# Optimization experiments

Measured on AMD Instinct MI355X. Metric: run time of the kernel, lower is better.

The kernel has to match this reference:

```python
import jax, jax.numpy as jnp
import numpy as np

N_NODES = 50000
N_EDGES = 800000
IN_C, HID_C, OUT_C = 128, 64, 40


def setup_inputs() -> dict:
    key = jax.random.key(0)
    ks = jax.random.split(key, 8)
    x = jax.random.normal(ks[0], (N_NODES, IN_C), dtype=jnp.float32)
    edge_index = jax.random.randint(ks[1], (2, N_EDGES), 0, N_NODES, dtype=jnp.int32)
    # Glorot-style init for the three GCNConv linear layers (bias zero as in PyG default reset)
    def glorot(k, fan_in, fan_out):
        lim = jnp.sqrt(6.0 / (fan_in + fan_out)).astype(jnp.float32)
        return jax.random.uniform(k, (fan_in, fan_out), dtype=jnp.float32, minval=-lim, maxval=lim)
    return {
        "x": x,
        "edge_index": edge_index,
        "W1": glorot(ks[2], IN_C, HID_C), "b1": jnp.zeros((HID_C,), jnp.float32),
        "W2": glorot(ks[3], HID_C, HID_C), "b2": jnp.zeros((HID_C,), jnp.float32),
        "W3": glorot(ks[4], HID_C, OUT_C), "b3": jnp.zeros((OUT_C,), jnp.float32),
    }


def _gcn_norm(edge_index, num_nodes):
    # PyG gcn_norm: add self-loops (weight 1), symmetric D^-1/2 (A+I) D^-1/2.
    loop = jnp.arange(num_nodes, dtype=edge_index.dtype)
    row = jnp.concatenate([edge_index[0], loop])  # source
    col = jnp.concatenate([edge_index[1], loop])  # target
    w = jnp.ones(row.shape[0], dtype=jnp.float32)
    deg = jax.ops.segment_sum(w, col, num_segments=num_nodes)
    dinv = jnp.where(deg > 0, jax.lax.rsqrt(deg), 0.0)
    norm = dinv[row] * w * dinv[col]  # [E+N]
    return row, col, norm


def _gcn_conv(x, row, col, norm, W, b):
    h = x @ W                         # linear first, as in PyG GCNConv
    msg = h[row] * norm[:, None]      # gather + scale  [E+N, F]
    agg = jax.ops.segment_sum(msg, col, num_segments=x.shape[0])
    return agg + b


def reference(x, edge_index, W1, b1, W2, b2, W3, b3):
    row, col, norm = _gcn_norm(edge_index, x.shape[0])
    h = jax.nn.relu(_gcn_conv(x, row, col, norm, W1, b1))   # dropout: eval-mode identity
    h = jax.nn.relu(_gcn_conv(h, row, col, norm, W2, b2))
    h = _gcn_conv(h, row, col, norm, W3, b3)
    return jax.nn.log_softmax(h, axis=-1)
```

## Files before the change

### kernel.cpp

```cpp
#include <hip/hip_runtime.h>
#include <hip/hip_bf16.h>
#include <math.h>


#define BSHIFT 10
#define CHUNK 2048
#define CAP 24576

__global__ __launch_bounds__(64) void tinyzero_kernel(int* __restrict__ p) {
  p[threadIdx.x] = 0;
}


__global__ __launch_bounds__(256) void bucketA_kernel(const int* __restrict__ row,
                                                      const int* __restrict__ col,
                                                      int* __restrict__ bcursor,
                                                      int2* __restrict__ tmp, int e) {
  __shared__ int bcnt[64], bstart[64], bbase[64];
  __shared__ int2 stage[CHUNK];
  int tid = threadIdx.x;
  int base = blockIdx.x * CHUNK;
  int cnt = e - base;
  if (cnt > CHUNK) cnt = CHUNK;
  if (tid < 64) bcnt[tid] = 0;
  __syncthreads();

  int2 ed[CHUNK / 256];
  int rk[CHUNK / 256];
#pragma unroll
  for (int k = 0; k < CHUNK / 256; ++k) {
    int j = tid + k * 256;
    if (j < cnt) {
      int c = col[base + j], r = row[base + j];
      ed[k] = make_int2(c, r);
      rk[k] = atomicAdd(&bcnt[c >> BSHIFT], 1);
    }
  }
  __syncthreads();
  if (tid < 64) {
    int v = bcnt[tid];
    int run = v;
#pragma unroll
    for (int off = 1; off < 64; off <<= 1) {
      int t = __shfl_up(run, off);
      if (tid >= off) run += t;
    }
    bstart[tid] = run - v;
    if (v > 0) bbase[tid] = atomicAdd(&bcursor[tid], v);
  }
  __syncthreads();
#pragma unroll
  for (int k = 0; k < CHUNK / 256; ++k) {
    int j = tid + k * 256;
    if (j < cnt) stage[bstart[ed[k].x >> BSHIFT] + rk[k]] = ed[k];
  }
  __syncthreads();
  for (int s = tid; s < cnt; s += 256) {
    int2 ev = stage[s];
    int b = ev.x >> BSHIFT;
    tmp[(size_t)b * CAP + bbase[b] + (s - bstart[b])] = ev;
  }
}


__global__ __launch_bounds__(256) void scatterB_kernel(const int2* __restrict__ tmp,
                                                       const int* __restrict__ bcursor,
                                                       int4* __restrict__ meta,
                                                       float* __restrict__ dinv,
                                                       int* __restrict__ csr, int n) {
  __shared__ int cnt[1 << BSHIFT];
  __shared__ int part[256];
  int tid = threadIdx.x;
  int b = blockIdx.x;
  int node0 = b << BSHIFT;
  int m = bcursor[b];
  const int2* src = tmp + (size_t)b * CAP;

  for (int t = tid; t < (1 << BSHIFT); t += 256) cnt[t] = 0;
  __syncthreads();
  for (int i = tid; i < m; i += 256)
    atomicAdd(&cnt[src[i].x & ((1 << BSHIFT) - 1)], 1);
  __syncthreads();

  int c0 = cnt[tid * 4 + 0], c1 = cnt[tid * 4 + 1];
  int c2 = cnt[tid * 4 + 2], c3 = cnt[tid * 4 + 3];
  int lsum = c0 + c1 + c2 + c3;
  part[tid] = lsum;
  __syncthreads();
#pragma unroll
  for (int off = 1; off < 256; off <<= 1) {
    int t = (tid >= off) ? part[tid - off] : 0;
    __syncthreads();
    part[tid] += t;
    __syncthreads();
  }
  int e0 = (tid == 0 ? 0 : part[tid - 1]);
  int e1 = e0 + c0, e2 = e1 + c1, e3 = e2 + c2;
  int base = b * CAP;

  int nd = node0 + tid * 4;
  if (nd + 0 < n) { float d = rsqrtf((float)(c0 + 1)); meta[nd + 0] = make_int4(base + e0, c0, __float_as_int(d), 0); dinv[nd + 0] = d; }
  if (nd + 1 < n) { float d = rsqrtf((float)(c1 + 1)); meta[nd + 1] = make_int4(base + e1, c1, __float_as_int(d), 0); dinv[nd + 1] = d; }
  if (nd + 2 < n) { float d = rsqrtf((float)(c2 + 1)); meta[nd + 2] = make_int4(base + e2, c2, __float_as_int(d), 0); dinv[nd + 2] = d; }
  if (nd + 3 < n) { float d = rsqrtf((float)(c3 + 1)); meta[nd + 3] = make_int4(base + e3, c3, __float_as_int(d), 0); dinv[nd + 3] = d; }
  __syncthreads();
  cnt[tid * 4 + 0] = e0; cnt[tid * 4 + 1] = e1;
  cnt[tid * 4 + 2] = e2; cnt[tid * 4 + 3] = e3;
  __syncthreads();

  for (int i = tid; i < m; i += 256) {
    int2 ev = src[i];
    int pos = atomicAdd(&cnt[ev.x & ((1 << BSHIFT) - 1)], 1);
    csr[base + pos] = ev.y;
  }
}


template <int K, int F>
__global__ __launch_bounds__(256) void gemm_kernel(const float* __restrict__ X,
                                                   const float* __restrict__ W,
                                                   const float* __restrict__ dinv,
                                                   __hip_bfloat16* __restrict__ Y, int n) {
  __shared__ float xs[16][K];
  int tid = threadIdx.x;
  int node0 = blockIdx.x * 16;
  constexpr int KV = K / 4;
  const float4* X4 = (const float4*)X;
  for (int i = tid; i < 16 * KV; i += 256) {
    int r = i / KV, c = i % KV;
    int nd = node0 + r;
    float4 v = make_float4(0.f, 0.f, 0.f, 0.f);
    if (nd < n) v = X4[(size_t)nd * KV + c];
    ((float4*)&xs[r][0])[c] = v;
  }
  __syncthreads();
  int g = tid >> 6, lane = tid & 63;
  if (lane < F) {
    float acc0 = 0.f, acc1 = 0.f, acc2 = 0.f, acc3 = 0.f;
#pragma unroll 8
    for (int k = 0; k < K; ++k) {
      float w = W[k * F + lane];
      acc0 += xs[g * 4 + 0][k] * w;
      acc1 += xs[g * 4 + 1][k] * w;
      acc2 += xs[g * 4 + 2][k] * w;
      acc3 += xs[g * 4 + 3][k] * w;
    }
    float accs[4] = {acc0, acc1, acc2, acc3};
#pragma unroll
    for (int j = 0; j < 4; ++j) {
      int nd = node0 + g * 4 + j;
      if (nd < n) Y[(size_t)nd * F + lane] = __float2bfloat16(accs[j] * dinv[nd]);
    }
  }
}


__device__ __forceinline__ float bflo(unsigned int u) {
  return __uint_as_float(u << 16);
}
__device__ __forceinline__ float bfhi(unsigned int u) {
  return __uint_as_float(u & 0xffff0000u);
}

template <int F, int MODE>
__global__ __launch_bounds__(256) void agg_kernel(const unsigned short* __restrict__ Hs,
                                                  const int* __restrict__ csr,
                                                  const int4* __restrict__ meta,
                                                  const float* __restrict__ bias,
                                                  float* __restrict__ Y, int n) {
  constexpr int FQ = F / 4;
  int wv = (blockIdx.x * 256 + threadIdx.x) >> 6;
  int lane = threadIdx.x & 63;
  int half = lane >> 5;
  int l32 = lane & 31;
  int sub = l32 >> 4;
  int fid = lane & 15;
  int node = wv * 2 + half;
  if (node >= n) return;
  bool activeF = (FQ == 16) || (fid < FQ);
  int hbase = 32 * half;

  int4 mt = meta[node];
  int s = mt.x, e = mt.x + mt.y;
  float di = __int_as_float(mt.z);

  float a0 = 0.f, a1 = 0.f, a2 = 0.f, a3 = 0.f;
  if (sub == 0 && activeF) {
    uint2 u = *(const uint2*)(Hs + (size_t)node * F + 4 * fid);
    a0 = bflo(u.x); a1 = bfhi(u.x); a2 = bflo(u.y); a3 = bfhi(u.y);
  }

  for (int base = s; base < e; base += 32) {
    int rem = e - base;
    int cnt = rem < 32 ? rem : 32;
    int p = csr[base + (l32 < cnt ? l32 : 0)];
    int j = 0;
    for (; j + 8 <= cnt; j += 8) {
      int r0 = __shfl(p, j + 0 + sub + hbase);
      int r1 = __shfl(p, j + 2 + sub + hbase);
      int r2 = __shfl(p, j + 4 + sub + hbase);
      int r3 = __shfl(p, j + 6 + sub + hbase);
      if (activeF) {
        uint2 u0 = *(const uint2*)(Hs + (size_t)r0 * F + 4 * fid);
        uint2 u1 = *(const uint2*)(Hs + (size_t)r1 * F + 4 * fid);
        uint2 u2 = *(const uint2*)(Hs + (size_t)r2 * F + 4 * fid);
        uint2 u3 = *(const uint2*)(Hs + (size_t)r3 * F + 4 * fid);
        a0 += bflo(u0.x); a1 += bfhi(u0.x); a2 += bflo(u0.y); a3 += bfhi(u0.y);
        a0 += bflo(u1.x); a1 += bfhi(u1.x); a2 += bflo(u1.y); a3 += bfhi(u1.y);
        a0 += bflo(u2.x); a1 += bfhi(u2.x); a2 += bflo(u2.y); a3 += bfhi(u2.y);
        a0 += bflo(u3.x); a1 += bfhi(u3.x); a2 += bflo(u3.y); a3 += bfhi(u3.y);
      }
    }
    for (; j < cnt; j += 2) {
      int idx = j + sub;
      int r = __shfl(p, (idx < cnt ? idx : j) + hbase);
      if (activeF && idx < cnt) {
        uint2 u = *(const uint2*)(Hs + (size_t)r * F + 4 * fid);
        a0 += bflo(u.x); a1 += bfhi(u.x); a2 += bflo(u.y); a3 += bfhi(u.y);
      }
    }
  }

  a0 += __shfl_xor(a0, 16);
  a1 += __shfl_xor(a1, 16);
  a2 += __shfl_xor(a2, 16);
  a3 += __shfl_xor(a3, 16);

  if (MODE == 0) {
    if (sub == 0 && activeF) {
      float4 bv = *(const float4*)(bias + 4 * fid);
      float v0 = a0 * di + bv.x, v1 = a1 * di + bv.y;
      float v2 = a2 * di + bv.z, v3 = a3 * di + bv.w;
      v0 = v0 > 0.f ? v0 : 0.f;
      v1 = v1 > 0.f ? v1 : 0.f;
      v2 = v2 > 0.f ? v2 : 0.f;
      v3 = v3 > 0.f ? v3 : 0.f;
      *(float4*)(Y + (size_t)node * F + 4 * fid) = make_float4(v0, v1, v2, v3);
    }
  } else {
    float v0 = -INFINITY, v1 = -INFINITY, v2 = -INFINITY, v3 = -INFINITY;
    if (activeF) {
      float4 bv = *(const float4*)(bias + 4 * fid);
      v0 = a0 * di + bv.x; v1 = a1 * di + bv.y;
      v2 = a2 * di + bv.z; v3 = a3 * di + bv.w;
    }
    float m = fmaxf(fmaxf(v0, v1), fmaxf(v2, v3));
#pragma unroll
    for (int off = 8; off; off >>= 1) m = fmaxf(m, __shfl_xor(m, off));
    float ex = 0.f;
    if (activeF)
      ex = expf(v0 - m) + expf(v1 - m) + expf(v2 - m) + expf(v3 - m);
#pragma unroll
    for (int off = 8; off; off >>= 1) ex += __shfl_xor(ex, off);
    float lg = m + logf(ex);
    if (sub == 0 && activeF) {
      *(float4*)(Y + (size_t)node * F + 4 * fid) =
          make_float4(v0 - lg, v1 - lg, v2 - lg, v3 - lg);
    }
  }
}


extern "C" void kernel_launch(void* const* d_in, const int* in_sizes, int n_in,
                              void* d_out, int out_size, void* d_ws, size_t ws_size,
                              hipStream_t stream) {
  const float* x  = (const float*)d_in[0];
  const int*   ei = (const int*)d_in[1];
  const float* W1 = (const float*)d_in[2];
  const float* b1 = (const float*)d_in[3];
  const float* W2 = (const float*)d_in[4];
  const float* b2 = (const float*)d_in[5];
  const float* W3 = (const float*)d_in[6];
  const float* b3 = (const float*)d_in[7];
  float* out = (float*)d_out;

  const int N = in_sizes[0] / 128;
  const int E = in_sizes[1] / 2;
  const int* erow = ei;
  const int* ecol = ei + E;

  const int nbuckets = (N + (1 << BSHIFT) - 1) >> BSHIFT;

  auto align_up = [](size_t v) { return (v + 255) & ~(size_t)255; };
  char* ws = (char*)d_ws;
  size_t off = 0;
  int* bcursor  = (int*)(ws + off); off += align_up(64 * 4);
  int4* meta    = (int4*)(ws + off); off += align_up((size_t)N * 16);
  float* dinv   = (float*)(ws + off); off += align_up((size_t)N * 4);
  int* csr      = (int*)(ws + off); off += align_up((size_t)nbuckets * CAP * 4);
  int2* tmp     = (int2*)(ws + off); off += align_up((size_t)nbuckets * CAP * 8);
  __hip_bfloat16* bufH = (__hip_bfloat16*)(ws + off); off += align_up((size_t)N * 64 * 2);
  float* bufF   = (float*)(ws + off); off += align_up((size_t)N * 64 * 4);
  (void)ws_size;

  const int cb = (E + CHUNK - 1) / CHUNK;

  tinyzero_kernel<<<1, 64, 0, stream>>>(bcursor);
  bucketA_kernel<<<cb, 256, 0, stream>>>(erow, ecol, bcursor, tmp, E);
  scatterB_kernel<<<nbuckets, 256, 0, stream>>>(tmp, bcursor, meta, dinv, csr, N);

  const int gemm_blocks = (N + 15) / 16;
  const int agg_blocks = (N + 7) / 8;

  gemm_kernel<128, 64><<<gemm_blocks, 256, 0, stream>>>(x, W1, dinv, bufH, N);
  agg_kernel<64, 0><<<agg_blocks, 256, 0, stream>>>((const unsigned short*)bufH, csr, meta, b1, bufF, N);

  gemm_kernel<64, 64><<<gemm_blocks, 256, 0, stream>>>(bufF, W2, dinv, bufH, N);
  agg_kernel<64, 0><<<agg_blocks, 256, 0, stream>>>((const unsigned short*)bufH, csr, meta, b2, bufF, N);

  gemm_kernel<64, 40><<<gemm_blocks, 256, 0, stream>>>(bufF, W3, dinv, bufH, N);
  agg_kernel<40, 1><<<agg_blocks, 256, 0, stream>>>((const unsigned short*)bufH, csr, meta, b3, out, N);
}
```

Baseline: 168.8 us.

## Fuse aggregation with next layer's linear transform via LDS staging

Merges each hidden-layer aggregation kernel with the following GEMM. Aggregated, biased and ReLU'd node rows go into shared memory, and each block then multiplies its 8 rows by the next weight matrix, writing bf16 output scaled by dinv. This drops two kernel launches and the fp32 intermediate write and read round trip. In exchange the in-block GEMM is a scalar loop that reads W from global memory per thread, and a block-wide barrier is added.

```diff
diff --git a/kernel.cpp b/kernel.cpp
--- a/kernel.cpp
+++ b/kernel.cpp
@@ -162,12 +162,108 @@
   return __uint_as_float(u & 0xffff0000u);
 }
 
-template <int F, int MODE>
-__global__ __launch_bounds__(256) void agg_kernel(const unsigned short* __restrict__ Hs,
-                                                  const int* __restrict__ csr,
-                                                  const int4* __restrict__ meta,
-                                                  const float* __restrict__ bias,
-                                                  float* __restrict__ Y, int n) {
+
+template <int FOUT>
+__global__ __launch_bounds__(256) void fused_agg_gemm_kernel(
+    const unsigned short* __restrict__ Hs, const int* __restrict__ csr,
+    const int4* __restrict__ meta, const float* __restrict__ bias,
+    const float* __restrict__ W, __hip_bfloat16* __restrict__ Yout, int n) {
+  constexpr int F = 64;
+  __shared__ float lds_x[8][F];
+  __shared__ float lds_di[8];
+  int tid = threadIdx.x;
+  int wv = (blockIdx.x * 256 + tid) >> 6;
+  int lane = tid & 63;
+  int half = lane >> 5;
+  int l32 = lane & 31;
+  int sub = l32 >> 4;
+  int fid = lane & 15;
+  int node = wv * 2 + half;
+  int nl = (tid >> 6) * 2 + half;
+  bool valid = node < n;
+
+  int s = 0, e = 0;
+  float di = 0.f;
+  if (valid) {
+    int4 mt = meta[node];
+    s = mt.x; e = mt.x + mt.y;
+    di = __int_as_float(mt.z);
+  }
+
+  float a0 = 0.f, a1 = 0.f, a2 = 0.f, a3 = 0.f;
+  if (valid && sub == 0) {
+    uint2 u = *(const uint2*)(Hs + (size_t)node * F + 4 * fid);
+    a0 = bflo(u.x); a1 = bfhi(u.x); a2 = bflo(u.y); a3 = bfhi(u.y);
+  }
+
+  int hbase = 32 * half;
+  for (int base = s; base < e; base += 32) {
+    int rem = e - base;
+    int cnt = rem < 32 ? rem : 32;
+    int p = csr[base + (l32 < cnt ? l32 : 0)];
+    int j = 0;
+    for (; j + 8 <= cnt; j += 8) {
+      int r0 = __shfl(p, j + 0 + sub + hbase);
+      int r1 = __shfl(p, j + 2 + sub + hbase);
+      int r2 = __shfl(p, j + 4 + sub + hbase);
+      int r3 = __shfl(p, j + 6 + sub + hbase);
+      uint2 u0 = *(const uint2*)(Hs + (size_t)r0 * F + 4 * fid);
+      uint2 u1 = *(const uint2*)(Hs + (size_t)r1 * F + 4 * fid);
+      uint2 u2 = *(const uint2*)(Hs + (size_t)r2 * F + 4 * fid);
+      uint2 u3 = *(const uint2*)(Hs + (size_t)r3 * F + 4 * fid);
+      a0 += bflo(u0.x); a1 += bfhi(u0.x); a2 += bflo(u0.y); a3 += bfhi(u0.y);
+      a0 += bflo(u1.x); a1 += bfhi(u1.x); a2 += bflo(u1.y); a3 += bfhi(u1.y);
+      a0 += bflo(u2.x); a1 += bfhi(u2.x); a2 += bflo(u2.y); a3 += bfhi(u2.y);
+      a0 += bflo(u3.x); a1 += bfhi(u3.x); a2 += bflo(u3.y); a3 += bfhi(u3.y);
+    }
+    for (; j < cnt; j += 2) {
+      int idx = j + sub;
+      int r = __shfl(p, (idx < cnt ? idx : j) + hbase);
+      if (idx < cnt) {
+        uint2 u = *(const uint2*)(Hs + (size_t)r * F + 4 * fid);
+        a0 += bflo(u.x); a1 += bfhi(u.x); a2 += bflo(u.y); a3 += bfhi(u.y);
+      }
+    }
+  }
+
+  a0 += __shfl_xor(a0, 16);
+  a1 += __shfl_xor(a1, 16);
+  a2 += __shfl_xor(a2, 16);
+  a3 += __shfl_xor(a3, 16);
+
+  if (valid && sub == 0) {
+    float4 bv = *(const float4*)(bias + 4 * fid);
+    float v0 = a0 * di + bv.x, v1 = a1 * di + bv.y;
+    float v2 = a2 * di + bv.z, v3 = a3 * di + bv.w;
+    v0 = v0 > 0.f ? v0 : 0.f;
+    v1 = v1 > 0.f ? v1 : 0.f;
+    v2 = v2 > 0.f ? v2 : 0.f;
+    v3 = v3 > 0.f ? v3 : 0.f;
+    ((float4*)&lds_x[nl][0])[fid] = make_float4(v0, v1, v2, v3);
+    if (fid == 0) lds_di[nl] = di;
+  }
+  __syncthreads();
+
+  int gn = tid >> 5;
+  int gnode = blockIdx.x * 8 + gn;
+  if (gnode < n) {
+    float gdi = lds_di[gn];
+    const float* xr = &lds_x[gn][0];
+    for (int fo = tid & 31; fo < FOUT; fo += 32) {
+      float acc = 0.f;
+#pragma unroll 8
+      for (int k = 0; k < F; ++k) acc += xr[k] * W[k * FOUT + fo];
+      Yout[(size_t)gnode * FOUT + fo] = __float2bfloat16(acc * gdi);
+    }
+  }
+}
+
+
+template <int F>
+__global__ __launch_bounds__(256) void agg_final_kernel(
+    const unsigned short* __restrict__ Hs, const int* __restrict__ csr,
+    const int4* __restrict__ meta, const float* __restrict__ bias,
+    float* __restrict__ Y, int n) {
   constexpr int FQ = F / 4;
   int wv = (blockIdx.x * 256 + threadIdx.x) >> 6;
   int lane = threadIdx.x & 63;
@@ -177,7 +273,7 @@
   int fid = lane & 15;
   int node = wv * 2 + half;
   if (node >= n) return;
-  bool activeF = (FQ == 16) || (fid < FQ);
+  bool activeF = fid < FQ;
   int hbase = 32 * half;
 
   int4 mt = meta[node];
@@ -226,37 +322,24 @@
   a2 += __shfl_xor(a2, 16);
   a3 += __shfl_xor(a3, 16);
 
-  if (MODE == 0) {
-    if (sub == 0 && activeF) {
-      float4 bv = *(const float4*)(bias + 4 * fid);
-      float v0 = a0 * di + bv.x, v1 = a1 * di + bv.y;
-      float v2 = a2 * di + bv.z, v3 = a3 * di + bv.w;
-      v0 = v0 > 0.f ? v0 : 0.f;
-      v1 = v1 > 0.f ? v1 : 0.f;
-      v2 = v2 > 0.f ? v2 : 0.f;
-      v3 = v3 > 0.f ? v3 : 0.f;
-      *(float4*)(Y + (size_t)node * F + 4 * fid) = make_float4(v0, v1, v2, v3);
-    }
-  } else {
-    float v0 = -INFINITY, v1 = -INFINITY, v2 = -INFINITY, v3 = -INFINITY;
-    if (activeF) {
-      float4 bv = *(const float4*)(bias + 4 * fid);
-      v0 = a0 * di + bv.x; v1 = a1 * di + bv.y;
-      v2 = a2 * di + bv.z; v3 = a3 * di + bv.w;
-    }
-    float m = fmaxf(fmaxf(v0, v1), fmaxf(v2, v3));
-#pragma unroll
-    for (int off = 8; off; off >>= 1) m = fmaxf(m, __shfl_xor(m, off));
-    float ex = 0.f;
-    if (activeF)
-      ex = expf(v0 - m) + expf(v1 - m) + expf(v2 - m) + expf(v3 - m);
-#pragma unroll
-    for (int off = 8; off; off >>= 1) ex += __shfl_xor(ex, off);
-    float lg = m + logf(ex);
-    if (sub == 0 && activeF) {
-      *(float4*)(Y + (size_t)node * F + 4 * fid) =
-          make_float4(v0 - lg, v1 - lg, v2 - lg, v3 - lg);
-    }
+  float v0 = -INFINITY, v1 = -INFINITY, v2 = -INFINITY, v3 = -INFINITY;
+  if (activeF) {
+    float4 bv = *(const float4*)(bias + 4 * fid);
+    v0 = a0 * di + bv.x; v1 = a1 * di + bv.y;
+    v2 = a2 * di + bv.z; v3 = a3 * di + bv.w;
+  }
+  float m = fmaxf(fmaxf(v0, v1), fmaxf(v2, v3));
+#pragma unroll
+  for (int off = 8; off; off >>= 1) m = fmaxf(m, __shfl_xor(m, off));
+  float ex = 0.f;
+  if (activeF)
+    ex = expf(v0 - m) + expf(v1 - m) + expf(v2 - m) + expf(v3 - m);
+#pragma unroll
+  for (int off = 8; off; off >>= 1) ex += __shfl_xor(ex, off);
+  float lg = m + logf(ex);
+  if (sub == 0 && activeF) {
+    *(float4*)(Y + (size_t)node * F + 4 * fid) =
+        make_float4(v0 - lg, v1 - lg, v2 - lg, v3 - lg);
   }
 }
 
@@ -289,8 +372,8 @@
   float* dinv   = (float*)(ws + off); off += align_up((size_t)N * 4);
   int* csr      = (int*)(ws + off); off += align_up((size_t)nbuckets * CAP * 4);
   int2* tmp     = (int2*)(ws + off); off += align_up((size_t)nbuckets * CAP * 8);
-  __hip_bfloat16* bufH = (__hip_bfloat16*)(ws + off); off += align_up((size_t)N * 64 * 2);
-  float* bufF   = (float*)(ws + off); off += align_up((size_t)N * 64 * 4);
+  __hip_bfloat16* bufA = (__hip_bfloat16*)(ws + off); off += align_up((size_t)N * 64 * 2);
+  __hip_bfloat16* bufB = (__hip_bfloat16*)(ws + off); off += align_up((size_t)N * 64 * 2);
   (void)ws_size;
 
   const int cb = (E + CHUNK - 1) / CHUNK;
@@ -300,14 +383,13 @@
   scatterB_kernel<<<nbuckets, 256, 0, stream>>>(tmp, bcursor, meta, dinv, csr, N);
 
   const int gemm_blocks = (N + 15) / 16;
-  const int agg_blocks = (N + 7) / 8;
-
-  gemm_kernel<128, 64><<<gemm_blocks, 256, 0, stream>>>(x, W1, dinv, bufH, N);
-  agg_kernel<64, 0><<<agg_blocks, 256, 0, stream>>>((const unsigned short*)bufH, csr, meta, b1, bufF, N);
-
-  gemm_kernel<64, 64><<<gemm_blocks, 256, 0, stream>>>(bufF, W2, dinv, bufH, N);
-  agg_kernel<64, 0><<<agg_blocks, 256, 0, stream>>>((const unsigned short*)bufH, csr, meta, b2, bufF, N);
-
-  gemm_kernel<64, 40><<<gemm_blocks, 256, 0, stream>>>(bufF, W3, dinv, bufH, N);
-  agg_kernel<40, 1><<<agg_blocks, 256, 0, stream>>>((const unsigned short*)bufH, csr, meta, b3, out, N);
-}
+  const int node8_blocks = (N + 7) / 8;
+
+  gemm_kernel<128, 64><<<gemm_blocks, 256, 0, stream>>>(x, W1, dinv, bufA, N);
+  fused_agg_gemm_kernel<64><<<node8_blocks, 256, 0, stream>>>(
+      (const unsigned short*)bufA, csr, meta, b1, W2, bufB, N);
+  fused_agg_gemm_kernel<40><<<node8_blocks, 256, 0, stream>>>(
+      (const unsigned short*)bufB, csr, meta, b2, W3, bufA, N);
+  agg_final_kernel<40><<<node8_blocks, 256, 0, stream>>>(
+      (const unsigned short*)bufA, csr, meta, b3, out, N);
+}
```

Result: slower. 179.3 us (+6.2%).
